# Kernel tuning notes

Measured on AMD Instinct MI355X. Metric: run time of the kernel, lower is better.

Reference implementation:

```python
import jax, jax.numpy as jnp
import numpy as np

T, N, D = 4096, 128, 128
NEG = -1.0e9


def setup_inputs() -> dict:
    key = jax.random.key(0)
    k1, k2, k3, k4 = jax.random.split(key, 4)
    return {
        "query": jax.random.normal(k1, (N, D), dtype=jnp.float32),
        "key": jax.random.normal(k2, (T, N, D), dtype=jnp.float32),
        "value": jax.random.normal(k3, (T, N, D), dtype=jnp.float32),
        "lens_for_attention": jax.random.randint(k4, (N,), 1, T + 1, dtype=jnp.int64 if jax.config.jax_enable_x64 else jnp.int32),
    }


def reference(query, key, value, lens_for_attention):
    # key, value: (T, N, D) -> (N, T, D)
    k = jnp.transpose(key, (1, 0, 2))
    v = jnp.transpose(value, (1, 0, 2))
    t = k.shape[1]
    # mask: True where timestep index >= length (padded positions)
    mask = jnp.arange(t)[None, :] >= lens_for_attention[:, None]  # (N, T)
    # energy = bmm(key, query): (N, T, D) @ (N, D) -> (N, T)
    energy = jnp.einsum('ntd,nd->nt', k, query)
    energy = jnp.where(mask, NEG, energy)
    attention = jax.nn.softmax(energy, axis=1)  # (N, T)
    # context = bmm(attention, value): (N, T) @ (N, T, D) -> (N, D)
    out = jnp.einsum('nt,ntd->nd', attention, v)
    return (out, attention)
```

## Files before the change

kernel.cpp:

```cpp
#include <hip/hip_runtime.h>

#define T_DIM 4096
#define N_DIM 128
#define D_DIM 128
#define CHUNK 256
#define NCHUNK (T_DIM / CHUNK)
#define NEGE (-1.0e9f)
#define P_SKIP 1.0e-9f

__global__ __launch_bounds__(256) void energy_kernel(
    const float* __restrict__ q,
    const float* __restrict__ key,
    const int*   __restrict__ lens,
    float*       __restrict__ att,
    float*       __restrict__ blockmax,
    float*       __restrict__ blocksum)
{
    const int b    = blockIdx.x;
    const int n    = b & (N_DIM - 1);
    const int c    = b >> 7;
    const int t0   = c * CHUNK;
    const int len  = lens[n];
    const int tid  = threadIdx.x;

    if (t0 >= len) {
        if (tid < 64)
            ((float4*)(att + (size_t)n * T_DIM + t0))[tid] =
                make_float4(NEGE, NEGE, NEGE, NEGE);
        if (tid == 0) {
            blockmax[n * NCHUNK + c] = NEGE;
            blocksum[n * NCHUNK + c] = 0.0f;
        }
        return;
    }

    const int wave = tid >> 6;
    const int lane = tid & 63;
    const int half = lane >> 5;
    const int l32  = lane & 31;

    const float4 qv = *(const float4*)(q + n * D_DIM + l32 * 4);

    float evals[CHUNK / 8];
    float lmax = NEGE;

    #pragma unroll
    for (int i = 0; i < CHUNK / 8; ++i) {
        const int t = t0 + wave * 2 + i * 8 + half;
        float e;
        if (t < len) {
            const float4 kv = *(const float4*)(key + (size_t)t * (N_DIM * D_DIM)
                                               + n * D_DIM + l32 * 4);
            float p = kv.x * qv.x + kv.y * qv.y + kv.z * qv.z + kv.w * qv.w;
            p += __shfl_xor(p, 1);
            p += __shfl_xor(p, 2);
            p += __shfl_xor(p, 4);
            p += __shfl_xor(p, 8);
            p += __shfl_xor(p, 16);
            e = p;
        } else {
            e = NEGE;
        }
        if (l32 == 0) att[(size_t)n * T_DIM + t] = e;
        evals[i] = e;
        lmax = fmaxf(lmax, e);
    }

    lmax = fmaxf(lmax, __shfl_xor(lmax, 32));
    __shared__ float smax[4];
    __shared__ float ssum[4];
    if (lane == 0) smax[wave] = lmax;
    __syncthreads();
    const float m = fmaxf(fmaxf(smax[0], smax[1]), fmaxf(smax[2], smax[3]));

    float s = 0.f;
    #pragma unroll
    for (int i = 0; i < CHUNK / 8; ++i) s += __expf(evals[i] - m);
    s += __shfl_xor(s, 32);
    if (lane == 0) ssum[wave] = s;
    __syncthreads();
    if (tid == 0) {
        blockmax[n * NCHUNK + c] = m;
        blocksum[n * NCHUNK + c] = ssum[0] + ssum[1] + ssum[2] + ssum[3];
    }
}

__global__ __launch_bounds__(256) void finalize_kernel(
    float*       __restrict__ att,
    const float* __restrict__ value,
    const float* __restrict__ blockmax,
    const float* __restrict__ blocksum,
    float*       __restrict__ out)
{
    const int n   = blockIdx.x;
    const int tid = threadIdx.x;

    __shared__ float sm[NCHUNK], ss[NCHUNK];
    __shared__ float sp[T_DIM];
    __shared__ int   slist[T_DIM];
    __shared__ int   scount;

    if (tid < NCHUNK) {
        sm[tid] = blockmax[n * NCHUNK + tid];
        ss[tid] = blocksum[n * NCHUNK + tid];
    }
    if (tid == 0) scount = 0;
    __syncthreads();

    float m = sm[0];
    #pragma unroll
    for (int i = 1; i < NCHUNK; ++i) m = fmaxf(m, sm[i]);
    float Z = 0.f;
    #pragma unroll
    for (int i = 0; i < NCHUNK; ++i) Z += ss[i] * __expf(sm[i] - m);
    const float inv = 1.0f / Z;

    float4* arow = (float4*)(att + (size_t)n * T_DIM);
    #pragma unroll
    for (int i = 0; i < T_DIM / 4 / 256; ++i) {
        const int idx = i * 256 + tid;
        float4 e4 = arow[idx];
        float4 p4;
        p4.x = __expf(e4.x - m) * inv;
        p4.y = __expf(e4.y - m) * inv;
        p4.z = __expf(e4.z - m) * inv;
        p4.w = __expf(e4.w - m) * inv;
        arow[idx] = p4;
        ((float4*)sp)[idx] = p4;
    }
    __syncthreads();

    for (int t = tid; t < T_DIM; t += 256) {
        if (sp[t] > P_SKIP) {
            const int j = atomicAdd(&scount, 1);
            slist[j] = t;
        }
    }
    __syncthreads();

    const int nc = scount;
    const int qd = tid & 31;
    const int g  = tid >> 5;
    float4 acc = make_float4(0.f, 0.f, 0.f, 0.f);
    for (int j = g; j < nc; j += 8) {
        const int t = slist[j];
        const float a = sp[t];
        const float4 v = *(const float4*)(value + (size_t)t * (N_DIM * D_DIM)
                                          + n * D_DIM + qd * 4);
        acc.x += a * v.x;
        acc.y += a * v.y;
        acc.z += a * v.z;
        acc.w += a * v.w;
    }

    __shared__ float4 buf[256];
    buf[tid] = acc;
    __syncthreads();
    if (tid < 128) {
        float4 o = buf[tid + 128];
        buf[tid].x += o.x; buf[tid].y += o.y; buf[tid].z += o.z; buf[tid].w += o.w;
    }
    __syncthreads();
    if (tid < 64) {
        float4 o = buf[tid + 64];
        buf[tid].x += o.x; buf[tid].y += o.y; buf[tid].z += o.z; buf[tid].w += o.w;
    }
    __syncthreads();
    if (tid < 32) {
        float4 a0 = buf[tid];
        float4 a1 = buf[tid + 32];
        ((float4*)(out + n * D_DIM))[tid] =
            make_float4(a0.x + a1.x, a0.y + a1.y, a0.z + a1.z, a0.w + a1.w);
    }
}

extern "C" void kernel_launch(void* const* d_in, const int* in_sizes, int n_in,
                              void* d_out, int out_size, void* d_ws, size_t ws_size,
                              hipStream_t stream) {
    const float* q     = (const float*)d_in[0];
    const float* key   = (const float*)d_in[1];
    const float* value = (const float*)d_in[2];
    const int*   lens  = (const int*)d_in[3];

    float* out = (float*)d_out;
    float* att = out + N_DIM * D_DIM;

    float* blockmax = (float*)d_ws;
    float* blocksum = (float*)((char*)d_ws + 8192);

    energy_kernel<<<N_DIM * NCHUNK, 256, 0, stream>>>(q, key, lens, att,
                                                      blockmax, blocksum);
    finalize_kernel<<<N_DIM, 256, 0, stream>>>(att, value,
                                               blockmax, blocksum, out);
}
```

Baseline: 471.0 us.

## Remap energy dot products per lane, widen finalize block, ballot-compact nonzero list

The energy kernel now gives each key row to 8 lanes, with each lane issuing four float4 loads. This raises memory-level parallelism and shortens the shuffle reduction. Energies are staged in shared memory for a coalesced row store and a single-pass max/sum reduction. The finalize kernel goes from 256 to 512 threads, so twice as many value rows are in flight per head. Its per-element atomic compaction becomes a wave ballot with one atomic per wave. Keys past the length inside a live chunk are now loaded unconditionally, which adds some wasted reads.

```diff
diff --git a/kernel.cpp b/kernel.cpp
--- a/kernel.cpp
+++ b/kernel.cpp
@@ -5,6 +5,7 @@
 #define D_DIM 128
 #define CHUNK 256
 #define NCHUNK (T_DIM / CHUNK)
+#define NDSZ   (N_DIM * D_DIM)
 #define NEGE (-1.0e9f)
 #define P_SKIP 1.0e-9f
 
@@ -34,58 +35,66 @@
         return;
     }
 
+    __shared__ float sEv[CHUNK];
+    __shared__ float sred[8];
+
     const int wave = tid >> 6;
     const int lane = tid & 63;
-    const int half = lane >> 5;
-    const int l32  = lane & 31;
-
-    const float4 qv = *(const float4*)(q + n * D_DIM + l32 * 4);
-
-    float evals[CHUNK / 8];
-    float lmax = NEGE;
-
-    #pragma unroll
-    for (int i = 0; i < CHUNK / 8; ++i) {
-        const int t = t0 + wave * 2 + i * 8 + half;
-        float e;
-        if (t < len) {
-            const float4 kv = *(const float4*)(key + (size_t)t * (N_DIM * D_DIM)
-                                               + n * D_DIM + l32 * 4);
-            float p = kv.x * qv.x + kv.y * qv.y + kv.z * qv.z + kv.w * qv.w;
-            p += __shfl_xor(p, 1);
-            p += __shfl_xor(p, 2);
-            p += __shfl_xor(p, 4);
-            p += __shfl_xor(p, 8);
-            p += __shfl_xor(p, 16);
-            e = p;
-        } else {
-            e = NEGE;
-        }
-        if (l32 == 0) att[(size_t)n * T_DIM + t] = e;
-        evals[i] = e;
-        lmax = fmaxf(lmax, e);
-    }
-
-    lmax = fmaxf(lmax, __shfl_xor(lmax, 32));
-    __shared__ float smax[4];
-    __shared__ float ssum[4];
-    if (lane == 0) smax[wave] = lmax;
-    __syncthreads();
-    const float m = fmaxf(fmaxf(smax[0], smax[1]), fmaxf(smax[2], smax[3]));
-
-    float s = 0.f;
-    #pragma unroll
-    for (int i = 0; i < CHUNK / 8; ++i) s += __expf(evals[i] - m);
+    const int dg   = lane & 7;
+    const int tg   = lane >> 3;
+
+    const float4* qp = (const float4*)(q + n * D_DIM) + dg;
+    const float4 q0 = qp[0], q1 = qp[8], q2 = qp[16], q3 = qp[24];
+
+    #pragma unroll
+    for (int it = 0; it < 8; ++it) {
+        const int t = t0 + wave * 64 + it * 8 + tg;
+        const float4* kp = (const float4*)(key + (size_t)t * NDSZ + n * D_DIM) + dg;
+        const float4 k0 = kp[0], k1 = kp[8], k2 = kp[16], k3 = kp[24];
+        float p = k0.x * q0.x + k0.y * q0.y + k0.z * q0.z + k0.w * q0.w;
+        p      += k1.x * q1.x + k1.y * q1.y + k1.z * q1.z + k1.w * q1.w;
+        p      += k2.x * q2.x + k2.y * q2.y + k2.z * q2.z + k2.w * q2.w;
+        p      += k3.x * q3.x + k3.y * q3.y + k3.z * q3.z + k3.w * q3.w;
+        p += __shfl_xor(p, 1);
+        p += __shfl_xor(p, 2);
+        p += __shfl_xor(p, 4);
+        const float e = (t < len) ? p : NEGE;
+        if (dg == 0) sEv[wave * 64 + it * 8 + tg] = e;
+    }
+    __syncthreads();
+
+    const float e = sEv[tid];
+    float m = e;
+    m = fmaxf(m, __shfl_xor(m, 1));
+    m = fmaxf(m, __shfl_xor(m, 2));
+    m = fmaxf(m, __shfl_xor(m, 4));
+    m = fmaxf(m, __shfl_xor(m, 8));
+    m = fmaxf(m, __shfl_xor(m, 16));
+    m = fmaxf(m, __shfl_xor(m, 32));
+    if (lane == 0) sred[wave] = m;
+    __syncthreads();
+    m = fmaxf(fmaxf(sred[0], sred[1]), fmaxf(sred[2], sred[3]));
+
+    float s = __expf(e - m);
+    s += __shfl_xor(s, 1);
+    s += __shfl_xor(s, 2);
+    s += __shfl_xor(s, 4);
+    s += __shfl_xor(s, 8);
+    s += __shfl_xor(s, 16);
     s += __shfl_xor(s, 32);
-    if (lane == 0) ssum[wave] = s;
+    if (lane == 0) sred[4 + wave] = s;
+
+    if (tid < 64)
+        ((float4*)(att + (size_t)n * T_DIM + t0))[tid] = ((const float4*)sEv)[tid];
+
     __syncthreads();
     if (tid == 0) {
         blockmax[n * NCHUNK + c] = m;
-        blocksum[n * NCHUNK + c] = ssum[0] + ssum[1] + ssum[2] + ssum[3];
+        blocksum[n * NCHUNK + c] = sred[4] + sred[5] + sred[6] + sred[7];
     }
 }
 
-__global__ __launch_bounds__(256) void finalize_kernel(
+__global__ __launch_bounds__(512) void finalize_kernel(
     float*       __restrict__ att,
     const float* __restrict__ value,
     const float* __restrict__ blockmax,
@@ -99,6 +108,7 @@
     __shared__ float sp[T_DIM];
     __shared__ int   slist[T_DIM];
     __shared__ int   scount;
+    __shared__ float4 buf[512];
 
     if (tid < NCHUNK) {
         sm[tid] = blockmax[n * NCHUNK + tid];
@@ -117,8 +127,8 @@
 
     float4* arow = (float4*)(att + (size_t)n * T_DIM);
     #pragma unroll
-    for (int i = 0; i < T_DIM / 4 / 256; ++i) {
-        const int idx = i * 256 + tid;
+    for (int i = 0; i < T_DIM / 4 / 512; ++i) {
+        const int idx = i * 512 + tid;
         float4 e4 = arow[idx];
         float4 p4;
         p4.x = __expf(e4.x - m) * inv;
@@ -130,10 +140,18 @@
     }
     __syncthreads();
 
-    for (int t = tid; t < T_DIM; t += 256) {
-        if (sp[t] > P_SKIP) {
-            const int j = atomicAdd(&scount, 1);
-            slist[j] = t;
+    const int lane = tid & 63;
+    #pragma unroll
+    for (int base = 0; base < T_DIM; base += 512) {
+        const int t = base + tid;
+        const bool pred = sp[t] > P_SKIP;
+        const unsigned long long mb = __ballot(pred);
+        int wbase = 0;
+        if (lane == 0) wbase = atomicAdd(&scount, __popcll(mb));
+        wbase = __shfl(wbase, 0);
+        if (pred) {
+            const int prefix = __popcll(mb & ((1ULL << lane) - 1));
+            slist[wbase + prefix] = t;
         }
     }
     __syncthreads();
@@ -142,10 +160,10 @@
     const int qd = tid & 31;
     const int g  = tid >> 5;
     float4 acc = make_float4(0.f, 0.f, 0.f, 0.f);
-    for (int j = g; j < nc; j += 8) {
+    for (int j = g; j < nc; j += 16) {
         const int t = slist[j];
         const float a = sp[t];
-        const float4 v = *(const float4*)(value + (size_t)t * (N_DIM * D_DIM)
+        const float4 v = *(const float4*)(value + (size_t)t * NDSZ
                                           + n * D_DIM + qd * 4);
         acc.x += a * v.x;
         acc.y += a * v.y;
@@ -153,19 +171,17 @@
         acc.w += a * v.w;
     }
 
-    __shared__ float4 buf[256];
     buf[tid] = acc;
     __syncthreads();
-    if (tid < 128) {
-        float4 o = buf[tid + 128];
-        buf[tid].x += o.x; buf[tid].y += o.y; buf[tid].z += o.z; buf[tid].w += o.w;
-    }
-    __syncthreads();
-    if (tid < 64) {
-        float4 o = buf[tid + 64];
-        buf[tid].x += o.x; buf[tid].y += o.y; buf[tid].z += o.z; buf[tid].w += o.w;
-    }
-    __syncthreads();
+    #pragma unroll
+    for (int off = 256; off > 32; off >>= 1) {
+        if (tid < off) {
+            float4 o = buf[tid + off];
+            buf[tid].x += o.x; buf[tid].y += o.y;
+            buf[tid].z += o.z; buf[tid].w += o.w;
+        }
+        __syncthreads();
+    }
     if (tid < 32) {
         float4 a0 = buf[tid];
         float4 a1 = buf[tid + 32];
@@ -190,6 +206,6 @@
 
     energy_kernel<<<N_DIM * NCHUNK, 256, 0, stream>>>(q, key, lens, att,
                                                       blockmax, blocksum);
-    finalize_kernel<<<N_DIM, 256, 0, stream>>>(att, value,
+    finalize_kernel<<<N_DIM, 512, 0, stream>>>(att, value,
                                                blockmax, blocksum, out);
 }
```

After: 457.4 us. -2.9%, faster.
